# Optimization experiments

Measured on AMD Instinct MI355X. Metric: run time of the kernel, lower is better.

The kernel has to match this reference:

```python
import jax, jax.numpy as jnp
import numpy as np
from jax import lax

B, N, C, D = 8, 512, 37, 2048          # frames, rois/frame, classes (incl. bg), feat dim
SCORE_THR = 0.1
NMS_THR = 0.4
BBOX_STDS = np.array([0.1, 0.1, 0.2, 0.2], dtype=np.float32)


def setup_inputs() -> dict:
    key = jax.random.key(0)
    k1, k2, k3, k4, k5, k6 = jax.random.split(key, 6)
    # rois: [batch_idx, x1, y1, x2, y2] in a 600x1000 image
    x1 = jax.random.uniform(k1, (B, N)) * 900.0
    y1 = jax.random.uniform(k2, (B, N)) * 500.0
    w = jax.random.uniform(k3, (B, N)) * 120.0 + 8.0
    h = jax.random.uniform(k4, (B, N)) * 120.0 + 8.0
    bidx = jnp.broadcast_to(jnp.arange(B, dtype=jnp.float32)[:, None], (B, N))
    rois = jnp.stack([bidx, x1, y1, x1 + w, y1 + h], axis=-1)  # [B,N,5]
    bbox_pred = jax.random.normal(k5, (B, N, 4 * C)) * 0.5
    scores = jax.nn.softmax(jax.random.normal(k6, (B, N, C)) * 2.0, axis=-1)
    im_info = jnp.tile(jnp.array([[600.0, 1000.0, 1.0]], dtype=jnp.float32), (B, 1))
    roi_features = jax.random.normal(jax.random.fold_in(key, 7), (B, N, D))
    return {"rois": rois, "bbox_pred": bbox_pred, "scores": scores,
            "im_info": im_info, "roi_features": roi_features}


def _iou_matrix(b):
    # b: [N,4] -> [N,N] pairwise IoU (torchvision nms convention, no +1)
    area = (b[:, 2] - b[:, 0]) * (b[:, 3] - b[:, 1])
    lt = jnp.maximum(b[:, None, :2], b[None, :, :2])
    rb = jnp.minimum(b[:, None, 2:], b[None, :, 2:])
    wh = jnp.clip(rb - lt, 0.0)
    inter = wh[..., 0] * wh[..., 1]
    return inter / (area[:, None] + area[None, :] - inter + 1e-9)


def _nms_one(boxes, scores):
    # boxes [N,4], scores [N] -> keep mask [N] (greedy NMS on score-thresholded boxes)
    n = boxes.shape[0]
    valid = scores > SCORE_THR
    order = jnp.argsort(-jnp.where(valid, scores, -jnp.inf))
    b = boxes[order]
    v = valid[order]
    iou = _iou_matrix(b)
    idx = jnp.arange(n)

    def body(i, keep):
        suppressed = jnp.any((iou[:, i] > NMS_THR) & keep & (idx < i))
        return keep.at[i].set(v[i] & ~suppressed)

    keep_sorted = lax.fori_loop(0, n, body, jnp.zeros(n, bool))
    return jnp.zeros(n, bool).at[order].set(keep_sorted)


def reference(rois, bbox_pred, scores, im_info, roi_features):
    stds = jnp.asarray(BBOX_STDS)
    deltas = bbox_pred.reshape(B, N, C, 4) * stds
    # bbox_transform_inv
    w = (rois[..., 3] - rois[..., 1])[..., None]             # [B,N,1]
    h = (rois[..., 4] - rois[..., 2])[..., None]
    cx = rois[..., 1][..., None] + 0.5 * w
    cy = rois[..., 2][..., None] + 0.5 * h
    px = deltas[..., 0] * w + cx
    py = deltas[..., 1] * h + cy
    pw = jnp.exp(deltas[..., 2]) * w
    ph = jnp.exp(deltas[..., 3]) * h
    x1 = px - 0.5 * pw
    y1 = py - 0.5 * ph
    x2 = px + 0.5 * pw
    y2 = py + 0.5 * ph
    # clip_boxes to image
    xmax = (im_info[:, 1] - 1.0)[:, None, None]
    ymax = (im_info[:, 0] - 1.0)[:, None, None]
    boxes = jnp.stack([jnp.clip(x1, 0.0, xmax), jnp.clip(y1, 0.0, ymax),
                       jnp.clip(x2, 0.0, xmax), jnp.clip(y2, 0.0, ymax)], axis=-1)  # [B,N,C,4]
    # foreground classes 1..C-1, class-major layout: [B,C-1,N,*]
    boxes_fg = jnp.moveaxis(boxes[:, :, 1:, :], 2, 1)        # [B,C-1,N,4]
    scores_fg = jnp.moveaxis(scores[:, :, 1:], 2, 1)         # [B,C-1,N]
    keep = jax.vmap(jax.vmap(_nms_one))(boxes_fg, scores_fg)  # [B,C-1,N] bool
    cls_dets = jnp.where(keep[..., None],
                         jnp.concatenate([boxes_fg, scores_fg[..., None]], axis=-1),
                         0.0)                                 # [B,C-1,N,5]
    kept_feats = jnp.where(jnp.any(keep, axis=1)[..., None], roi_features, 0.0)  # [B,N,D]
    return cls_dets, kept_feats, keep
```

## Files before the change

kernel.cpp:

```cpp
#include <hip/hip_runtime.h>
#include <math.h>

#define BATCH 8
#define BN    512
#define NC    37
#define NFG   36
#define FD    2048


__global__ __launch_bounds__(256) void nms_kernel(
    const float* __restrict__ rois,
    const float* __restrict__ bbox_pred,
    const float* __restrict__ scores,
    const float* __restrict__ im_info,
    float* __restrict__ cls_dets,
    float* __restrict__ keep_out)
{
    const int bc  = blockIdx.x;
    const int b   = bc / NFG;
    const int cc  = bc % NFG;
    const int c   = cc + 1;
    const int tid = threadIdx.x;

    __shared__ float sb[BN][4];
    __shared__ float sarea[BN];
    __shared__ float skey[BN];
    __shared__ int   sidx[BN];
    __shared__ unsigned char srem[BN];
    __shared__ int   sV;

    if (tid == 0) sV = 0;
    __syncthreads();

    const float xmax = im_info[b * 3 + 1] - 1.0f;
    const float ymax = im_info[b * 3 + 0] - 1.0f;

    int vcnt = 0;
    for (int n = tid; n < BN; n += 256) {
        const float* r = rois + (size_t)(b * BN + n) * 5;
        const float x1r = r[1], y1r = r[2], x2r = r[3], y2r = r[4];
        const float w  = x2r - x1r;
        const float h  = y2r - y1r;
        const float cx = x1r + 0.5f * w;
        const float cy = y1r + 0.5f * h;
        const float* dp = bbox_pred + (size_t)(b * BN + n) * (4 * NC) + 4 * c;
        const float dx  = dp[0] * 0.1f;
        const float dy  = dp[1] * 0.1f;
        const float dlw = dp[2] * 0.2f;
        const float dlh = dp[3] * 0.2f;
        const float px = dx * w + cx;
        const float py = dy * h + cy;
        const float pw = expf(dlw) * w;
        const float ph = expf(dlh) * h;
        float bx1 = px - 0.5f * pw;
        float by1 = py - 0.5f * ph;
        float bx2 = px + 0.5f * pw;
        float by2 = py + 0.5f * ph;
        bx1 = fminf(fmaxf(bx1, 0.0f), xmax);
        by1 = fminf(fmaxf(by1, 0.0f), ymax);
        bx2 = fminf(fmaxf(bx2, 0.0f), xmax);
        by2 = fminf(fmaxf(by2, 0.0f), ymax);
        sb[n][0] = bx1; sb[n][1] = by1; sb[n][2] = bx2; sb[n][3] = by2;
        sarea[n] = (bx2 - bx1) * (by2 - by1);
        const float s = scores[(size_t)(b * BN + n) * NC + c];
        const bool valid = s > 0.1f;
        skey[n] = valid ? s : -INFINITY;
        sidx[n] = n;
        if (valid) vcnt++;
    }
    atomicAdd(&sV, vcnt);

    for (unsigned k = 2; k <= BN; k <<= 1) {
        for (unsigned j = k >> 1; j > 0; j >>= 1) {
            __syncthreads();
            for (unsigned i = tid; i < BN; i += 256) {
                const unsigned ixj = i ^ j;
                if (ixj > i) {
                    const float ka = skey[i], kb = skey[ixj];
                    const int   ia = sidx[i], ib = sidx[ixj];
                    const bool a_first = (ka > kb) || (ka == kb && ia < ib);
                    const bool up = ((i & k) == 0);
                    const bool do_swap = up ? !a_first : a_first;
                    if (do_swap) {
                        skey[i] = kb; skey[ixj] = ka;
                        sidx[i] = ib; sidx[ixj] = ia;
                    }
                }
            }
        }
    }
    __syncthreads();

    const int V = sV;
    for (int i = tid; i < BN; i += 256) srem[i] = (i < V) ? 1 : 0;

    for (int i = 0; i < V; ++i) {
        __syncthreads();
        if (!srem[i]) continue;
        const int   ni  = sidx[i];
        const float ax1 = sb[ni][0], ay1 = sb[ni][1];
        const float ax2 = sb[ni][2], ay2 = sb[ni][3];
        const float aar = sarea[ni];
        for (int jj = tid; jj < V; jj += 256) {
            if (jj > i && srem[jj]) {
                const int nj = sidx[jj];
                const float ix1 = fmaxf(ax1, sb[nj][0]);
                const float iy1 = fmaxf(ay1, sb[nj][1]);
                const float ix2 = fminf(ax2, sb[nj][2]);
                const float iy2 = fminf(ay2, sb[nj][3]);
                const float iw = fmaxf(ix2 - ix1, 0.0f);
                const float ih = fmaxf(iy2 - iy1, 0.0f);
                const float inter = iw * ih;
                const float iou = inter / (aar + sarea[nj] - inter + 1e-9f);
                if (iou > 0.4f) srem[jj] = 0;
            }
        }
    }
    __syncthreads();

    for (int i = tid; i < BN; i += 256) {
        const int n    = sidx[i];
        const int kept = srem[i];
        const size_t obase = (size_t)(b * NFG + cc) * BN + n;
        keep_out[obase] = kept ? 1.0f : 0.0f;
        float* cd = cls_dets + obase * 5;
        if (kept) {
            cd[0] = sb[n][0]; cd[1] = sb[n][1];
            cd[2] = sb[n][2]; cd[3] = sb[n][3];
            cd[4] = skey[i];
        } else {
            cd[0] = 0.0f; cd[1] = 0.0f; cd[2] = 0.0f; cd[3] = 0.0f; cd[4] = 0.0f;
        }
    }
}

__global__ __launch_bounds__(256) void feat_kernel(
    const float* __restrict__ feats,
    const float* __restrict__ keepf,
    float* __restrict__ out_feats)
{
    const int bn = blockIdx.x;
    const int b  = bn >> 9;
    const int n  = bn & (BN - 1);

    __shared__ int s_any;
    if (threadIdx.x == 0) s_any = 0;
    __syncthreads();
    if (threadIdx.x < NFG) {
        if (keepf[((size_t)b * NFG + threadIdx.x) * BN + n] != 0.0f)
            s_any = 1;
    }
    __syncthreads();
    const float m = s_any ? 1.0f : 0.0f;

    const float4* src = (const float4*)(feats + (size_t)(b * BN + n) * FD);
    float4*       dst = (float4*)(out_feats + (size_t)(b * BN + n) * FD);
    for (int t = threadIdx.x; t < FD / 4; t += 256) {
        float4 v = src[t];
        dst[t] = make_float4(v.x * m, v.y * m, v.z * m, v.w * m);
    }
}

extern "C" void kernel_launch(void* const* d_in, const int* in_sizes, int n_in,
                              void* d_out, int out_size, void* d_ws, size_t ws_size,
                              hipStream_t stream) {
    const float* rois      = (const float*)d_in[0];
    const float* bbox_pred = (const float*)d_in[1];
    const float* scores    = (const float*)d_in[2];
    const float* im_info   = (const float*)d_in[3];
    const float* feats     = (const float*)d_in[4];

    float* out        = (float*)d_out;
    float* cls_dets   = out;
    float* kept_feats = out + (size_t)BATCH * NFG * BN * 5;
    float* keep_out   = kept_feats + (size_t)BATCH * BN * FD;

    nms_kernel<<<BATCH * NFG, 256, 0, stream>>>(rois, bbox_pred, scores, im_info,
                                                cls_dets, keep_out);
    feat_kernel<<<BATCH * BN, 256, 0, stream>>>(feats, keep_out, kept_feats);
}
```

Baseline: 136.1 us.

## Compact valid boxes with ballot and run single-wavefront register NMS

```diff
diff --git a/kernel.cpp b/kernel.cpp
--- a/kernel.cpp
+++ b/kernel.cpp
@@ -8,156 +8,205 @@
 #define FD    2048
 
 
-__global__ __launch_bounds__(256) void nms_kernel(
+__global__ __launch_bounds__(64) void nms_kernel(
     const float* __restrict__ rois,
     const float* __restrict__ bbox_pred,
     const float* __restrict__ scores,
     const float* __restrict__ im_info,
     float* __restrict__ cls_dets,
-    float* __restrict__ keep_out)
+    float* __restrict__ keep_out,
+    int*   __restrict__ anykeep)
 {
-    const int bc  = blockIdx.x;
-    const int b   = bc / NFG;
-    const int cc  = bc % NFG;
-    const int c   = cc + 1;
-    const int tid = threadIdx.x;
+    const int bc   = blockIdx.x;
+    const int b    = bc / NFG;
+    const int cc   = bc % NFG;
+    const int c    = cc + 1;
+    const int lane = threadIdx.x;
 
     __shared__ float sb[BN][4];
     __shared__ float sarea[BN];
-    __shared__ float skey[BN];
-    __shared__ int   sidx[BN];
+    __shared__ float cscore[BN];
+    __shared__ int   cn[BN];
+    __shared__ float kflag[BN];
     __shared__ unsigned char srem[BN];
-    __shared__ int   sV;
-
-    if (tid == 0) sV = 0;
-    __syncthreads();
 
     const float xmax = im_info[b * 3 + 1] - 1.0f;
     const float ymax = im_info[b * 3 + 0] - 1.0f;
-
-    int vcnt = 0;
-    for (int n = tid; n < BN; n += 256) {
-        const float* r = rois + (size_t)(b * BN + n) * 5;
-        const float x1r = r[1], y1r = r[2], x2r = r[3], y2r = r[4];
-        const float w  = x2r - x1r;
-        const float h  = y2r - y1r;
-        const float cx = x1r + 0.5f * w;
-        const float cy = y1r + 0.5f * h;
-        const float* dp = bbox_pred + (size_t)(b * BN + n) * (4 * NC) + 4 * c;
-        const float dx  = dp[0] * 0.1f;
-        const float dy  = dp[1] * 0.1f;
-        const float dlw = dp[2] * 0.2f;
-        const float dlh = dp[3] * 0.2f;
-        const float px = dx * w + cx;
-        const float py = dy * h + cy;
-        const float pw = expf(dlw) * w;
-        const float ph = expf(dlh) * h;
-        float bx1 = px - 0.5f * pw;
-        float by1 = py - 0.5f * ph;
-        float bx2 = px + 0.5f * pw;
-        float by2 = py + 0.5f * ph;
-        bx1 = fminf(fmaxf(bx1, 0.0f), xmax);
-        by1 = fminf(fmaxf(by1, 0.0f), ymax);
-        bx2 = fminf(fmaxf(bx2, 0.0f), xmax);
-        by2 = fminf(fmaxf(by2, 0.0f), ymax);
-        sb[n][0] = bx1; sb[n][1] = by1; sb[n][2] = bx2; sb[n][3] = by2;
-        sarea[n] = (bx2 - bx1) * (by2 - by1);
-        const float s = scores[(size_t)(b * BN + n) * NC + c];
-        const bool valid = s > 0.1f;
-        skey[n] = valid ? s : -INFINITY;
-        sidx[n] = n;
-        if (valid) vcnt++;
-    }
-    atomicAdd(&sV, vcnt);
-
-    for (unsigned k = 2; k <= BN; k <<= 1) {
-        for (unsigned j = k >> 1; j > 0; j >>= 1) {
-            __syncthreads();
-            for (unsigned i = tid; i < BN; i += 256) {
-                const unsigned ixj = i ^ j;
-                if (ixj > i) {
-                    const float ka = skey[i], kb = skey[ixj];
-                    const int   ia = sidx[i], ib = sidx[ixj];
-                    const bool a_first = (ka > kb) || (ka == kb && ia < ib);
-                    const bool up = ((i & k) == 0);
-                    const bool do_swap = up ? !a_first : a_first;
-                    if (do_swap) {
-                        skey[i] = kb; skey[ixj] = ka;
-                        sidx[i] = ib; sidx[ixj] = ia;
+    const unsigned long long lmask_lt = (lane == 0) ? 0ull : ((1ull << lane) - 1ull);
+
+    float sc[8];
+#pragma unroll
+    for (int r = 0; r < 8; ++r) {
+        const int n = r * 64 + lane;
+        sc[r] = scores[(size_t)(b * BN + n) * NC + c];
+        kflag[n] = 0.0f;
+    }
+    int base = 0;
+#pragma unroll
+    for (int r = 0; r < 8; ++r) {
+        const int n = r * 64 + lane;
+        const bool valid = sc[r] > 0.1f;
+        const unsigned long long m = __ballot(valid);
+        if (valid) {
+            const int pos = base + __popcll(m & lmask_lt);
+            cscore[pos] = sc[r];
+            cn[pos] = n;
+            const float* rr = rois + (size_t)(b * BN + n) * 5;
+            const float x1r = rr[1], y1r = rr[2], x2r = rr[3], y2r = rr[4];
+            const float w  = x2r - x1r;
+            const float h  = y2r - y1r;
+            const float cx = x1r + 0.5f * w;
+            const float cy = y1r + 0.5f * h;
+            const float* dp = bbox_pred + (size_t)(b * BN + n) * (4 * NC) + 4 * c;
+            const float px = (dp[0] * 0.1f) * w + cx;
+            const float py = (dp[1] * 0.1f) * h + cy;
+            const float pw = expf(dp[2] * 0.2f) * w;
+            const float ph = expf(dp[3] * 0.2f) * h;
+            float bx1 = fminf(fmaxf(px - 0.5f * pw, 0.0f), xmax);
+            float by1 = fminf(fmaxf(py - 0.5f * ph, 0.0f), ymax);
+            float bx2 = fminf(fmaxf(px + 0.5f * pw, 0.0f), xmax);
+            float by2 = fminf(fmaxf(py + 0.5f * ph, 0.0f), ymax);
+            sb[n][0] = bx1; sb[n][1] = by1; sb[n][2] = bx2; sb[n][3] = by2;
+            sarea[n] = (bx2 - bx1) * (by2 - by1);
+        }
+        base += __popcll(m);
+    }
+    const int V = base;
+    __syncthreads();
+
+    if (V <= 64) {
+        float key; int id;
+        if (lane < V) { key = cscore[lane]; id = cn[lane]; }
+        else          { key = -INFINITY;    id = BN + lane; }
+#pragma unroll
+        for (int k = 2; k <= 64; k <<= 1) {
+#pragma unroll
+            for (int j = k >> 1; j > 0; j >>= 1) {
+                const float ok = __shfl_xor(key, j);
+                const int   oi = __shfl_xor(id, j);
+                const bool is_lower   = (lane & j) == 0;
+                const bool dir_desc   = (lane & k) == 0;
+                const bool mine_first = (key > ok) || (key == ok && id < oi);
+                bool take = mine_first ^ is_lower;
+                if (!dir_desc) take = !take;
+                if (take) { key = ok; id = oi; }
+            }
+        }
+        float x1 = 0, y1 = 0, x2 = 0, y2 = 0, ar = 0;
+        if (lane < V) { x1 = sb[id][0]; y1 = sb[id][1]; x2 = sb[id][2]; y2 = sb[id][3]; ar = sarea[id]; }
+        unsigned long long rem = (V == 64) ? ~0ull : ((1ull << V) - 1ull);
+        for (int i = 0; i < V; ++i) {
+            if (!((rem >> i) & 1ull)) continue;
+            const float ax1 = __shfl(x1, i);
+            const float ay1 = __shfl(y1, i);
+            const float ax2 = __shfl(x2, i);
+            const float ay2 = __shfl(y2, i);
+            const float aar = __shfl(ar, i);
+            const float ix1 = fmaxf(ax1, x1);
+            const float iy1 = fmaxf(ay1, y1);
+            const float ix2 = fminf(ax2, x2);
+            const float iy2 = fminf(ay2, y2);
+            const float iw = fmaxf(ix2 - ix1, 0.0f);
+            const float ih = fmaxf(iy2 - iy1, 0.0f);
+            const float inter = iw * ih;
+            const float iou = inter / (aar + ar - inter + 1e-9f);
+            const unsigned long long sup = __ballot((iou > 0.4f) && (lane > i));
+            rem &= ~sup;
+        }
+        if (lane < V && ((rem >> lane) & 1ull)) {
+            kflag[id] = key;
+            anykeep[b * BN + id] = 1;
+        }
+    } else {
+        int P = 64; while (P < V) P <<= 1;
+        for (int i = lane; i < P; i += 64) {
+            if (i >= V) { cscore[i] = -INFINITY; cn[i] = BN + i; }
+            srem[i] = (i < V) ? 1 : 0;
+        }
+        __syncthreads();
+        for (int k = 2; k <= P; k <<= 1) {
+            for (int j = k >> 1; j > 0; j >>= 1) {
+                __syncthreads();
+                for (int i = lane; i < P; i += 64) {
+                    const int ixj = i ^ j;
+                    if (ixj > i) {
+                        const float ka = cscore[i], kb = cscore[ixj];
+                        const int   ia = cn[i],     ib = cn[ixj];
+                        const bool a_first = (ka > kb) || (ka == kb && ia < ib);
+                        const bool up = ((i & k) == 0);
+                        if (up ? !a_first : a_first) {
+                            cscore[i] = kb; cscore[ixj] = ka;
+                            cn[i] = ib;     cn[ixj] = ia;
+                        }
                     }
                 }
             }
         }
+        __syncthreads();
+        for (int i = 0; i < V; ++i) {
+            __syncthreads();
+            if (!srem[i]) continue;
+            const int   ni  = cn[i];
+            const float ax1 = sb[ni][0], ay1 = sb[ni][1];
+            const float ax2 = sb[ni][2], ay2 = sb[ni][3];
+            const float aar = sarea[ni];
+            for (int jj = lane; jj < V; jj += 64) {
+                if (jj > i && srem[jj]) {
+                    const int nj = cn[jj];
+                    const float ix1 = fmaxf(ax1, sb[nj][0]);
+                    const float iy1 = fmaxf(ay1, sb[nj][1]);
+                    const float ix2 = fminf(ax2, sb[nj][2]);
+                    const float iy2 = fminf(ay2, sb[nj][3]);
+                    const float iw = fmaxf(ix2 - ix1, 0.0f);
+                    const float ih = fmaxf(iy2 - iy1, 0.0f);
+                    const float inter = iw * ih;
+                    const float iou = inter / (aar + sarea[nj] - inter + 1e-9f);
+                    if (iou > 0.4f) srem[jj] = 0;
+                }
+            }
+        }
+        __syncthreads();
+        for (int i = lane; i < V; i += 64) {
+            if (srem[i]) {
+                kflag[cn[i]] = cscore[i];
+                anykeep[b * BN + cn[i]] = 1;
+            }
+        }
     }
     __syncthreads();
 
-    const int V = sV;
-    for (int i = tid; i < BN; i += 256) srem[i] = (i < V) ? 1 : 0;
-
-    for (int i = 0; i < V; ++i) {
-        __syncthreads();
-        if (!srem[i]) continue;
-        const int   ni  = sidx[i];
-        const float ax1 = sb[ni][0], ay1 = sb[ni][1];
-        const float ax2 = sb[ni][2], ay2 = sb[ni][3];
-        const float aar = sarea[ni];
-        for (int jj = tid; jj < V; jj += 256) {
-            if (jj > i && srem[jj]) {
-                const int nj = sidx[jj];
-                const float ix1 = fmaxf(ax1, sb[nj][0]);
-                const float iy1 = fmaxf(ay1, sb[nj][1]);
-                const float ix2 = fminf(ax2, sb[nj][2]);
-                const float iy2 = fminf(ay2, sb[nj][3]);
-                const float iw = fmaxf(ix2 - ix1, 0.0f);
-                const float ih = fmaxf(iy2 - iy1, 0.0f);
-                const float inter = iw * ih;
-                const float iou = inter / (aar + sarea[nj] - inter + 1e-9f);
-                if (iou > 0.4f) srem[jj] = 0;
-            }
-        }
-    }
-    __syncthreads();
-
-    for (int i = tid; i < BN; i += 256) {
-        const int n    = sidx[i];
-        const int kept = srem[i];
-        const size_t obase = (size_t)(b * NFG + cc) * BN + n;
-        keep_out[obase] = kept ? 1.0f : 0.0f;
-        float* cd = cls_dets + obase * 5;
-        if (kept) {
-            cd[0] = sb[n][0]; cd[1] = sb[n][1];
-            cd[2] = sb[n][2]; cd[3] = sb[n][3];
-            cd[4] = skey[i];
-        } else {
-            cd[0] = 0.0f; cd[1] = 0.0f; cd[2] = 0.0f; cd[3] = 0.0f; cd[4] = 0.0f;
-        }
+    const size_t rowbase = (size_t)(b * NFG + cc) * BN;
+#pragma unroll
+    for (int r = 0; r < 8; ++r) {
+        const int n = r * 64 + lane;
+        const float s = kflag[n];
+        const bool kept = s > 0.0f;
+        keep_out[rowbase + n] = kept ? 1.0f : 0.0f;
+        float* cd = cls_dets + (rowbase + n) * 5;
+        cd[0] = kept ? sb[n][0] : 0.0f;
+        cd[1] = kept ? sb[n][1] : 0.0f;
+        cd[2] = kept ? sb[n][2] : 0.0f;
+        cd[3] = kept ? sb[n][3] : 0.0f;
+        cd[4] = kept ? s : 0.0f;
     }
 }
 
 __global__ __launch_bounds__(256) void feat_kernel(
     const float* __restrict__ feats,
-    const float* __restrict__ keepf,
+    const int*   __restrict__ anykeep,
     float* __restrict__ out_feats)
 {
     const int bn = blockIdx.x;
-    const int b  = bn >> 9;
-    const int n  = bn & (BN - 1);
-
-    __shared__ int s_any;
-    if (threadIdx.x == 0) s_any = 0;
-    __syncthreads();
-    if (threadIdx.x < NFG) {
-        if (keepf[((size_t)b * NFG + threadIdx.x) * BN + n] != 0.0f)
-            s_any = 1;
-    }
-    __syncthreads();
-    const float m = s_any ? 1.0f : 0.0f;
-
-    const float4* src = (const float4*)(feats + (size_t)(b * BN + n) * FD);
-    float4*       dst = (float4*)(out_feats + (size_t)(b * BN + n) * FD);
-    for (int t = threadIdx.x; t < FD / 4; t += 256) {
-        float4 v = src[t];
-        dst[t] = make_float4(v.x * m, v.y * m, v.z * m, v.w * m);
+    const int flag = anykeep[bn];
+    const float4* src = (const float4*)(feats + (size_t)bn * FD);
+    float4*       dst = (float4*)(out_feats + (size_t)bn * FD);
+    if (flag) {
+#pragma unroll
+        for (int t = threadIdx.x; t < FD / 4; t += 256) dst[t] = src[t];
+    } else {
+        const float4 z = make_float4(0.f, 0.f, 0.f, 0.f);
+#pragma unroll
+        for (int t = threadIdx.x; t < FD / 4; t += 256) dst[t] = z;
     }
 }
 
@@ -175,7 +224,10 @@
     float* kept_feats = out + (size_t)BATCH * NFG * BN * 5;
     float* keep_out   = kept_feats + (size_t)BATCH * BN * FD;
 
-    nms_kernel<<<BATCH * NFG, 256, 0, stream>>>(rois, bbox_pred, scores, im_info,
-                                                cls_dets, keep_out);
-    feat_kernel<<<BATCH * BN, 256, 0, stream>>>(feats, keep_out, kept_feats);
+    int* anykeep = (int*)d_ws;
+    hipMemsetAsync(anykeep, 0, (size_t)BATCH * BN * sizeof(int), stream);
+
+    nms_kernel<<<BATCH * NFG, 64, 0, stream>>>(rois, bbox_pred, scores, im_info,
+                                               cls_dets, keep_out, anykeep);
+    feat_kernel<<<BATCH * BN, 256, 0, stream>>>(feats, anykeep, kept_feats);
 }
```

Result: faster. 112.1 us (-17.7%).
